# Kernel optimization log

Measured on AMD Instinct MI355X. Metric: run time of the kernel, lower is better.

The kernel has to match this reference:

```python
import jax, jax.numpy as jnp
import numpy as np

B, N, E, H, T, L, NH = 256, 200, 1600, 256, 30, 30, 4
DH = H // NH


def setup_inputs() -> dict:
    key = jax.random.key(0)
    ks = jax.random.split(key, 24)
    s = 0.05
    nrm = lambda k, shape, sc=s: jax.random.normal(k, shape, jnp.float32) * sc
    return {
        'x_feats': nrm(ks[0], (5, B, T, 2), 1.0),
        'node_features': nrm(ks[1], (B, N, 4), 1.0),
        'edge_index': jax.random.randint(ks[2], (B, 2, E), 0, N),
        'gcn_W1': nrm(ks[3], (4, H)),
        'gcn_b1': nrm(ks[4], (H,)),
        'gcn_W2': nrm(ks[5], (H, H)),
        'gcn_b2': nrm(ks[6], (H,)),
        'attn_in_w': nrm(ks[7], (3 * H, H)),
        'attn_in_b': nrm(ks[8], (3 * H,)),
        'attn_out_w': nrm(ks[9], (H, H)),
        'attn_out_b': nrm(ks[10], (H,)),
        'Wih0': nrm(ks[11], (5, 4 * H, 2 + H)),
        'Wih1': nrm(ks[12], (5, 4 * H, H)),
        'Whh': nrm(ks[13], (5, 2, 4 * H, H)),
        'bih': nrm(ks[14], (5, 2, 4 * H)),
        'bhh': nrm(ks[15], (5, 2, 4 * H)),
        'fcW_pv': nrm(ks[16], (2, 2 * L, H)),
        'fcb_pv': nrm(ks[17], (2, 2 * L)),
        'fcW_s': nrm(ks[18], (3, L, H)),
        'fcb_s': nrm(ks[19], (3, L)),
    }


def _lstm2(xin, Wih0, Wih1, Whh, bih, bhh):
    # xin: [B, T, D]; 2-layer LSTM (PyTorch gate order i, f, g, o). Returns last hidden [B, H].
    def run_layer(xt, Wih, Whh_l, b):  # xt: [T, B, D]
        def step(carry, x_t):
            h, c = carry
            z = x_t @ Wih.T + h @ Whh_l.T + b
            i, f, g, o = jnp.split(z, 4, axis=-1)
            c = jax.nn.sigmoid(f) * c + jax.nn.sigmoid(i) * jnp.tanh(g)
            h = jax.nn.sigmoid(o) * jnp.tanh(c)
            return (h, c), h
        z0 = jnp.zeros((xt.shape[1], H), xt.dtype)
        _, ys = jax.lax.scan(step, (z0, z0), xt)
        return ys  # [T, B, H]

    y0 = run_layer(xin.transpose(1, 0, 2), Wih0, Whh[0], bih[0] + bhh[0])
    y1 = run_layer(y0, Wih1, Whh[1], bih[1] + bhh[1])
    return y1[-1]  # [B, H]


def reference(x_feats, node_features, edge_index, gcn_W1, gcn_b1, gcn_W2, gcn_b2,
              attn_in_w, attn_in_b, attn_out_w, attn_out_b,
              Wih0, Wih1, Whh, bih, bhh, fcW_pv, fcb_pv, fcW_s, fcb_s):
    # --- per-graph 2-layer GCN (symmetric-normalized, self-loops), vmapped over batch ---
    def gcn_graph(x, ei):  # x: [N, 4], ei: [2, E]
        ar = jnp.arange(N)
        src = jnp.concatenate([ei[0], ar])
        tgt = jnp.concatenate([ei[1], ar])
        deg = jax.ops.segment_sum(jnp.ones_like(src, dtype=x.dtype), tgt, num_segments=N)
        dinv = jnp.where(deg > 0, jax.lax.rsqrt(deg), 0.0)
        norm = (dinv[src] * dinv[tgt])[:, None]
        def conv(h, W, b):
            m = h @ W
            return jax.ops.segment_sum(norm * m[src], tgt, num_segments=N) + b
        h = jax.nn.relu(conv(x, gcn_W1, gcn_b1))
        return jax.nn.relu(conv(h, gcn_W2, gcn_b2))

    g = jax.vmap(gcn_graph)(node_features, edge_index)  # [B, N, H]

    # --- multi-head self-attention over the N node axis ---
    qkv = g @ attn_in_w.T + attn_in_b  # [B, N, 3H]
    q, k, v = jnp.split(qkv, 3, axis=-1)
    q = q.reshape(B, N, NH, DH)
    k = k.reshape(B, N, NH, DH)
    v = v.reshape(B, N, NH, DH)
    scores = jnp.einsum('bqhd,bkhd->bhqk', q, k) / jnp.sqrt(jnp.asarray(DH, g.dtype))
    attn = jax.nn.softmax(scores, axis=-1)
    o = jnp.einsum('bhqk,bkhd->bqhd', attn, v).reshape(B, N, H)
    o = o @ attn_out_w.T + attn_out_b  # [B, N, H]
    gfeat = o.mean(axis=1)  # mean over node/seq axis -> [B, H]

    # --- broadcast graph context to each timestep, concat with per-branch features ---
    g_rep = jnp.broadcast_to(gfeat[None, :, None, :], (5, B, T, H))
    branch_in = jnp.concatenate([x_feats, g_rep], axis=-1)  # [5, B, T, 2+H]

    # --- 5 branch LSTMs, vmapped over the branch axis ---
    last_h = jax.vmap(_lstm2)(branch_in, Wih0, Wih1, Whh, bih, bhh)  # [5, B, H]

    # --- heads ---
    pv = jnp.einsum('kbh,koh->kbo', last_h[:2], fcW_pv) + fcb_pv[:, None, :]  # [2, B, 2L]
    position_pred = pv[0].reshape(B, L, 2)
    velocity_pred = pv[1].reshape(B, L, 2)
    sot = jnp.einsum('kbh,koh->kbo', last_h[2:], fcW_s) + fcb_s[:, None, :]  # [3, B, L]
    steering_pred = sot[0][..., None]
    object_pred = jax.nn.sigmoid(sot[1])[..., None]
    traffic_pred = jax.nn.sigmoid(sot[2])[..., None]
    # concat heads along last axis: [B, L, 2+2+1+1+1]
    return jnp.concatenate([position_pred, velocity_pred, steering_pred, object_pred, traffic_pred], axis=-1)
```

## Files before the change

### kernel.cpp

```cpp
#include <hip/hip_runtime.h>
#include <hip/hip_bf16.h>

typedef __hip_bfloat16 bf16;
typedef __bf16 bh8 __attribute__((ext_vector_type(8)));
typedef float f32x4 __attribute__((ext_vector_type(4)));

#define BBATCH 256
#define NN   200
#define EE   1600

#define GLOAD16(gp, lp) __builtin_amdgcn_global_load_lds( \
    (const __attribute__((address_space(1))) void*)(gp),  \
    (__attribute__((address_space(3))) void*)(lp), 16, 0, 0)

__device__ inline float bf2f(bf16 v) { return __bfloat162float(v); }
__device__ inline float ldf(const float* p) { return *p; }
__device__ inline float ldf(const bf16* p) { return __bfloat162float(*p); }
__device__ inline void stf(float* p, float v) { *p = v; }
__device__ inline void stf(bf16* p, float v) { *p = __float2bfloat16(v); }

__global__ __launch_bounds__(256) void k_diag(float* out, int n, float v) {
    for (int i = blockIdx.x * 256 + threadIdx.x; i < n; i += gridDim.x * 256) out[i] = v;
}

__global__ __launch_bounds__(256) void k_deg(const int* __restrict__ ei, int* __restrict__ cnt) {
    int idx = blockIdx.x * 256 + threadIdx.x;
    int b = idx / EE, e = idx % EE;
    int tg = ei[(long)b * 2 * EE + EE + e];
    atomicAdd(&cnt[b * NN + tg], 1);
}

__global__ __launch_bounds__(256) void k_dinv(const int* __restrict__ cnt, float* __restrict__ dinv) {
    int i = blockIdx.x * 256 + threadIdx.x;
    dinv[i] = rsqrtf((float)cnt[i] + 1.0f);
}

__global__ __launch_bounds__(256) void k_adj(const int* __restrict__ ei, const float* __restrict__ dinv,
                                             float* __restrict__ AdjF) {
    int idx = blockIdx.x * 256 + threadIdx.x;
    int b = idx / EE, e = idx % EE;
    const int* eb = ei + (long)b * 2 * EE;
    int s = eb[e], tg = eb[EE + e];
    atomicAdd(&AdjF[((long)b * NN + tg) * NN + s], dinv[b * NN + tg] * dinv[b * NN + s]);
}

__global__ __launch_bounds__(256) void k_adjself(const float* __restrict__ dinv, float* __restrict__ AdjF) {
    int idx = blockIdx.x * 256 + threadIdx.x;
    int b = idx / NN, n = idx % NN;
    float d = dinv[idx];
    atomicAdd(&AdjF[((long)b * NN + n) * NN + n], d * d);
}

__global__ __launch_bounds__(256) void k_adjconv(const float* __restrict__ AdjF, bf16* __restrict__ Adjb) {
    long idx = (long)blockIdx.x * 256 + threadIdx.x;
    int col = idx % 224;
    int row = (idx / 224) & 255;
    int b = idx / (224 * 256);
    float v = (row < NN && col < NN) ? AdjF[((long)b * NN + row) * NN + col] : 0.f;
    Adjb[idx] = __float2bfloat16(v);
}

__global__ __launch_bounds__(256) void k_m1t(const float* __restrict__ nf, const float* __restrict__ W1,
                                             bf16* __restrict__ m1t) {
    long idx = (long)blockIdx.x * 256 + threadIdx.x;
    int node = idx % 224;
    int h = (idx / 224) & 255;
    int b = idx / (224 * 256);
    float v = 0.f;
    if (node < NN) {
        const float* x = nf + ((long)b * NN + node) * 4;
        v = x[0] * W1[h] + x[1] * W1[256 + h] + x[2] * W1[512 + h] + x[3] * W1[768 + h];
    }
    m1t[idx] = __float2bfloat16(v);
}

__global__ __launch_bounds__(256) void k_conv(const float* __restrict__ s, bf16* __restrict__ d, int n) {
    int i = blockIdx.x * 256 + threadIdx.x;
    if (i < n) d[i] = __float2bfloat16(s[i]);
}

__global__ __launch_bounds__(256) void k_convT(const float* __restrict__ W2, bf16* __restrict__ w2t) {
    int i = blockIdx.x * 256 + threadIdx.x;
    w2t[i] = __float2bfloat16(W2[((i & 255) << 8) + (i >> 8)]);
}

__global__ __launch_bounds__(256) void k_bsum(const float* __restrict__ bih, const float* __restrict__ bhh,
                                              float* __restrict__ bsum) {
    int i = blockIdx.x * 256 + threadIdx.x;
    bsum[i] = bih[i] + bhh[i];
}

__global__ __launch_bounds__(256) void k_wfrag(const float* __restrict__ Whh, bf16* __restrict__ dst_, int layer) {
    int i = blockIdx.x * 256 + threadIdx.x;
    int lane = i & 63, g = (i >> 6) & 3, kc = (i >> 8) & 7, jw = (i >> 11) & 15, br = i >> 15;
    int row = g * 256 + jw * 16 + (lane & 15);
    int col = kc * 32 + (lane >> 4) * 8;
    const float* src = Whh + (long)(br * 2 + layer) * 262144 + (long)row * 256 + col;
    bf16* dst = dst_ + (long)i * 8;
#pragma unroll
    for (int e = 0; e < 8; ++e) dst[e] = __float2bfloat16(src[e]);
}

template<int BM, int BN, bool RELU, bool CT>
__global__ __launch_bounds__(256)
void mgemm(const bf16* __restrict__ A, long aBatch, int lda,
           const bf16* __restrict__ Bt, long bBatch, int ldb,
           bf16* __restrict__ C, long cBatch, int ldc,
           const float* __restrict__ bias, long biasBatch,
           int K, int Mvalid)
{
    constexpr int ACH = BM / 16, TCH = BM / 16 + BN / 16, PW = TCH / 4;
    constexpr int FM = BM / 32, FN = BN / 32;
    __shared__ bf16 Al[BM][32];
    __shared__ bf16 Bl[BN][32];
    int bz = blockIdx.z;
    const bf16* Ab = A + (long)bz * aBatch + (long)blockIdx.y * BM * lda;
    const bf16* Bb = Bt + (long)bz * bBatch + (long)blockIdx.x * BN * ldb;
    int tid = threadIdx.x, w = tid >> 6, l = tid & 63;
    int wm = w >> 1, wn = w & 1;
    int lrow = l >> 2, lk8 = (l & 3) * 8;
    f32x4 acc[FM][FN] = {};
    for (int k0 = 0; k0 < K; k0 += 32) {
#pragma unroll
        for (int cc = 0; cc < PW; ++cc) {
            int c = w * PW + cc;
            if (c < ACH) GLOAD16(Ab + (long)(c * 16 + lrow) * lda + k0 + lk8, ((char*)&Al[0][0]) + c * 1024);
            else { int bc = c - ACH; GLOAD16(Bb + (long)(bc * 16 + lrow) * ldb + k0 + lk8, ((char*)&Bl[0][0]) + bc * 1024); }
        }
        __syncthreads();
        bh8 af[FM], bfv[FN];
#pragma unroll
        for (int i = 0; i < FM; ++i) af[i] = *(const bh8*)&Al[wm * (BM / 2) + i * 16 + (l & 15)][(l >> 4) * 8];
#pragma unroll
        for (int j = 0; j < FN; ++j) bfv[j] = *(const bh8*)&Bl[wn * (BN / 2) + j * 16 + (l & 15)][(l >> 4) * 8];
#pragma unroll
        for (int i = 0; i < FM; ++i)
#pragma unroll
            for (int j = 0; j < FN; ++j)
                acc[i][j] = __builtin_amdgcn_mfma_f32_16x16x32_bf16(af[i], bfv[j], acc[i][j], 0, 0, 0);
        __syncthreads();
    }
    bf16* Cb = C + (long)bz * cBatch;
    int mq = blockIdx.y * BM + wm * (BM / 2);
    int nq = blockIdx.x * BN + wn * (BN / 2);
#pragma unroll
    for (int i = 0; i < FM; ++i) {
#pragma unroll
        for (int j = 0; j < FN; ++j) {
            int n = nq + j * 16 + (l & 15);
            float bv = bias ? bias[(long)bz * biasBatch + n] : 0.f;
            int m0 = mq + i * 16 + (l >> 4) * 4;
#pragma unroll
            for (int r = 0; r < 4; ++r) {
                int m = m0 + r;
                if (m < Mvalid) {
                    float v = acc[i][j][r] + bv;
                    if (RELU) v = fmaxf(v, 0.f);
                    if (CT) Cb[(long)n * ldc + m] = __float2bfloat16(v);
                    else    Cb[(long)m * ldc + n] = __float2bfloat16(v);
                }
            }
        }
    }
}

__global__ __launch_bounds__(1024)
void k_rnn0(const bf16* __restrict__ wfrag0, const bf16* __restrict__ gpart,
            const float* __restrict__ xf, const float* __restrict__ wih0,
            bf16* __restrict__ y0)
{
    __shared__ bf16 hbuf[2][16][256];
    int g_ = 10 * (blockIdx.x & 7) + (blockIdx.x >> 3);
    int btile = g_ & 15, br = g_ >> 4;
    int tid = threadIdx.x, w = tid >> 6, l = tid & 63;
    int ln = l & 15, lg = l >> 4;
    int j = w * 16 + ln;
    const bf16* wb = wfrag0 + ((long)(br * 16 + w)) * 16384 + l * 8;
    float2 w01[4];
    float gp_c[4][4];
#pragma unroll
    for (int g = 0; g < 4; ++g) {
        w01[g] = *(const float2*)(wih0 + ((long)br * 1024 + g * 256 + j) * 258);
#pragma unroll
        for (int r = 0; r < 4; ++r) {
            int b = btile * 16 + lg * 4 + r;
            gp_c[g][r] = bf2f(gpart[((long)br * 256 + b) * 1024 + g * 256 + j]);
        }
    }
    float c[4] = {};
    int pp = 0;
#pragma unroll 1
    for (int t = 0; t < 30; ++t) {
        f32x4 acc[4] = {};
        if (t > 0) {
            const char* hb = (const char*)hbuf[pp ^ 1];
#pragma unroll
            for (int kc = 0; kc < 8; ++kc) {
                bh8 a = *(const bh8*)(hb + ln * 512 + ((kc * 64 + lg * 16) ^ ((ln & 7) << 4)));
                const bf16* wk = wb + kc * 2048;
#pragma unroll
                for (int g = 0; g < 4; ++g)
                    acc[g] = __builtin_amdgcn_mfma_f32_16x16x32_bf16(a, *(const bh8*)(wk + g * 512), acc[g], 0, 0, 0);
            }
        }
        char* hw = (char*)hbuf[pp];
        float2 xr[4];
#pragma unroll
        for (int r = 0; r < 4; ++r) {
            int b = btile * 16 + lg * 4 + r;
            xr[r] = *(const float2*)(xf + ((long)(br * 256 + b) * 30 + t) * 2);
        }
#pragma unroll
        for (int r = 0; r < 4; ++r) {
            float z[4];
#pragma unroll
            for (int g = 0; g < 4; ++g)
                z[g] = acc[g][r] + gp_c[g][r] + xr[r].x * w01[g].x + xr[r].y * w01[g].y;
            float ig = 1.f / (1.f + __expf(-z[0]));
            float fg = 1.f / (1.f + __expf(-z[1]));
            float gv = 2.f / (1.f + __expf(-2.f * z[2])) - 1.f;
            float og = 1.f / (1.f + __expf(-z[3]));
            float cv = fg * c[r] + ig * gv;
            c[r] = cv;
            float hv = og * (2.f / (1.f + __expf(-2.f * cv)) - 1.f);
            int row = lg * 4 + r;
            *(bf16*)(hw + row * 512 + ((2 * j) ^ ((row & 7) << 4))) = __float2bfloat16(hv);
        }
        __syncthreads();
        {
            int row = tid >> 6;
            int off = (tid & 63) * 8;
            uint2 v = *(const uint2*)(hw + row * 512 + (off ^ ((row & 7) << 4)));
            *(uint2*)((char*)y0 + (((long)(br * 30 + t) * 256 + btile * 16 + row) * 512) + off) = v;
        }
        pp ^= 1;
    }
}

__global__ __launch_bounds__(1024)
void k_rnn1(const bf16* __restrict__ wfrag1, const bf16* __restrict__ zin1,
            bf16* __restrict__ h1out)
{
    __shared__ bf16 hbuf[2][16][256];
    int g_ = 10 * (blockIdx.x & 7) + (blockIdx.x >> 3);
    int btile = g_ & 15, br = g_ >> 4;
    int tid = threadIdx.x, w = tid >> 6, l = tid & 63;
    int ln = l & 15, lg = l >> 4;
    int j = w * 16 + ln;
    const bf16* wb = wfrag1 + ((long)(br * 16 + w)) * 16384 + l * 8;
    float c[4] = {};
    int pp = 0;
    const bf16* zbr = zin1 + (long)br * 7864320;
#pragma unroll 1
    for (int t = 0; t < 30; ++t) {
        float zin[4][4];
#pragma unroll
        for (int r = 0; r < 4; ++r) {
            long mrow = (long)(t * 256 + btile * 16 + lg * 4 + r) * 1024;
#pragma unroll
            for (int g = 0; g < 4; ++g) zin[g][r] = bf2f(zbr[mrow + g * 256 + j]);
        }
        f32x4 acc[4] = {};
        if (t > 0) {
            const char* hb = (const char*)hbuf[pp ^ 1];
#pragma unroll
            for (int kc = 0; kc < 8; ++kc) {
                bh8 a = *(const bh8*)(hb + ln * 512 + ((kc * 64 + lg * 16) ^ ((ln & 7) << 4)));
                const bf16* wk = wb + kc * 2048;
#pragma unroll
                for (int g = 0; g < 4; ++g)
                    acc[g] = __builtin_amdgcn_mfma_f32_16x16x32_bf16(a, *(const bh8*)(wk + g * 512), acc[g], 0, 0, 0);
            }
        }
        char* hw = (char*)hbuf[pp];
#pragma unroll
        for (int r = 0; r < 4; ++r) {
            float z[4];
#pragma unroll
            for (int g = 0; g < 4; ++g) z[g] = acc[g][r] + zin[g][r];
            float ig = 1.f / (1.f + __expf(-z[0]));
            float fg = 1.f / (1.f + __expf(-z[1]));
            float gv = 2.f / (1.f + __expf(-2.f * z[2])) - 1.f;
            float og = 1.f / (1.f + __expf(-z[3]));
            float cv = fg * c[r] + ig * gv;
            c[r] = cv;
            float hv = og * (2.f / (1.f + __expf(-2.f * cv)) - 1.f);
            int row = lg * 4 + r;
            *(bf16*)(hw + row * 512 + ((2 * j) ^ ((row & 7) << 4))) = __float2bfloat16(hv);
            if (t == 29) {
                int b = btile * 16 + row;
                h1out[((long)br * 256 + b) * 256 + j] = __float2bfloat16(hv);
            }
        }
        __syncthreads();
        pp ^= 1;
    }
}

template <bool BT, typename TA, typename TB, typename TC>
__global__ __launch_bounds__(256)
void gemm64(const TA* __restrict__ A, long aBatch, int lda,
            const TB* __restrict__ Bm, long bBatch, int ldb,
            TC* __restrict__ C, long cBatch, int ldc,
            const float* __restrict__ bias, long biasBatch,
            int M, int Nn, int K, int flags) {
    __shared__ float As[16][64];
    __shared__ float Bs[16][64];
    int bz = blockIdx.z;
    const TA* Ab = A + (long)bz * aBatch;
    const TB* Bb = Bm + (long)bz * bBatch;
    TC* Cb = C + (long)bz * cBatch;
    int m0 = blockIdx.y * 64, n0 = blockIdx.x * 64;
    int tid = threadIdx.x;
    int tr = tid >> 4, tc = tid & 15;
    float acc[4][4] = {};
    int la_m = tid >> 2;
    int la_k = (tid & 3) * 4;
    for (int k0 = 0; k0 < K; k0 += 16) {
#pragma unroll
        for (int j = 0; j < 4; ++j) {
            int kk = la_k + j;
            float v = 0.f;
            if (m0 + la_m < M && k0 + kk < K) v = ldf(&Ab[(long)(m0 + la_m) * lda + k0 + kk]);
            As[kk][la_m] = v;
        }
        if (!BT) {
            int n = tid & 63, kb = (tid >> 6) * 4;
#pragma unroll
            for (int j = 0; j < 4; ++j) {
                int kk = kb + j;
                float v = 0.f;
                if (k0 + kk < K && n0 + n < Nn) v = ldf(&Bb[(long)(k0 + kk) * ldb + n0 + n]);
                Bs[kk][n] = v;
            }
        } else {
            int n = tid >> 2, kb = (tid & 3) * 4;
#pragma unroll
            for (int j = 0; j < 4; ++j) {
                int kk = kb + j;
                float v = 0.f;
                if (k0 + kk < K && n0 + n < Nn) v = ldf(&Bb[(long)(n0 + n) * ldb + k0 + kk]);
                Bs[kk][n] = v;
            }
        }
        __syncthreads();
#pragma unroll
        for (int kk = 0; kk < 16; ++kk) {
            float4 a4 = *(const float4*)&As[kk][tr * 4];
            float4 b4 = *(const float4*)&Bs[kk][tc * 4];
            float a[4] = {a4.x, a4.y, a4.z, a4.w};
            float bb[4] = {b4.x, b4.y, b4.z, b4.w};
#pragma unroll
            for (int i = 0; i < 4; ++i)
#pragma unroll
                for (int j = 0; j < 4; ++j) acc[i][j] += a[i] * bb[j];
        }
        __syncthreads();
    }
#pragma unroll
    for (int i = 0; i < 4; ++i) {
        int m = m0 + tr * 4 + i;
        if (m >= M) continue;
#pragma unroll
        for (int j = 0; j < 4; ++j) {
            int n = n0 + tc * 4 + j;
            if (n >= Nn) continue;
            float v = acc[i][j];
            if (bias) v += bias[(long)bz * biasBatch + n];
            if (flags & 1) v = fmaxf(v, 0.f);
            stf(&Cb[(long)m * ldc + n], v);
        }
    }
}

__global__ __launch_bounds__(256) void k_attn(const bf16* __restrict__ qkv, float* __restrict__ gmean) {
    int b = blockIdx.x >> 2, hd = blockIdx.x & 3;
    __shared__ bf16 Ks[208][72];
    __shared__ float CSl[4][208];
    __shared__ float Gp[4][64];
    int tid = threadIdx.x, w = tid >> 6, l = tid & 63;
    const bf16* qb = qkv + (long)b * (NN * 768) + hd * 64;
    for (int i = tid; i < 208 * 8; i += 256) {
        int n = i >> 3, g = i & 7;
        uint4 v = make_uint4(0, 0, 0, 0);
        if (n < NN) v = *(const uint4*)(qb + (long)n * 768 + 256 + g * 8);
        *(uint4*)&Ks[n][g * 8] = v;
    }
    __syncthreads();
    float cs[13];
#pragma unroll
    for (int t = 0; t < 13; ++t) cs[t] = 0.f;
    int ln = l & 15, lg = l >> 4;
    for (int qt = w; qt < 13; qt += 4) {
        int qr = qt * 16 + ln; if (qr > NN - 1) qr = NN - 1;
        bh8 aq0 = *(const bh8*)(qb + (long)qr * 768 + lg * 8);
        bh8 aq1 = *(const bh8*)(qb + (long)qr * 768 + 32 + lg * 8);
        f32x4 s[13];
#pragma unroll
        for (int t = 0; t < 13; ++t) s[t] = f32x4{0.f, 0.f, 0.f, 0.f};
#pragma unroll
        for (int t = 0; t < 13; ++t) {
            bh8 b0 = *(const bh8*)&Ks[t * 16 + ln][lg * 8];
            bh8 b1 = *(const bh8*)&Ks[t * 16 + ln][32 + lg * 8];
            s[t] = __builtin_amdgcn_mfma_f32_16x16x32_bf16(aq0, b0, s[t], 0, 0, 0);
            s[t] = __builtin_amdgcn_mfma_f32_16x16x32_bf16(aq1, b1, s[t], 0, 0, 0);
        }
        float mx[4] = {-1e30f, -1e30f, -1e30f, -1e30f};
#pragma unroll
        for (int t = 0; t < 13; ++t) {
            bool vn = (t < 12) | (ln < 8);
#pragma unroll
            for (int r = 0; r < 4; ++r) {
                float v = s[t][r] * 0.125f;
                s[t][r] = v;
                if (vn) mx[r] = fmaxf(mx[r], v);
            }
        }
#pragma unroll
        for (int off = 1; off < 16; off <<= 1)
#pragma unroll
            for (int r = 0; r < 4; ++r) mx[r] = fmaxf(mx[r], __shfl_xor(mx[r], off));
        float sum[4] = {0.f, 0.f, 0.f, 0.f};
#pragma unroll
        for (int t = 0; t < 13; ++t) {
            bool vn = (t < 12) | (ln < 8);
#pragma unroll
            for (int r = 0; r < 4; ++r) {
                float e = vn ? __expf(s[t][r] - mx[r]) : 0.f;
                s[t][r] = e;
                sum[r] += e;
            }
        }
#pragma unroll
        for (int off = 1; off < 16; off <<= 1)
#pragma unroll
            for (int r = 0; r < 4; ++r) sum[r] += __shfl_xor(sum[r], off);
        float inv[4];
#pragma unroll
        for (int r = 0; r < 4; ++r) inv[r] = 1.f / sum[r];
#pragma unroll
        for (int r = 0; r < 4; ++r) {
            int q = qt * 16 + lg * 4 + r;
            if (q < NN) {
#pragma unroll
                for (int t = 0; t < 13; ++t) cs[t] += s[t][r] * inv[r];
            }
        }
    }
#pragma unroll
    for (int t = 0; t < 13; ++t) {
        cs[t] += __shfl_xor(cs[t], 16);
        cs[t] += __shfl_xor(cs[t], 32);
    }
    if (l < 16) {
#pragma unroll
        for (int t = 0; t < 13; ++t) CSl[w][t * 16 + l] = cs[t];
    }
    __syncthreads();
    float part = 0.f;
    for (int n = w * 50; n < w * 50 + 50; ++n) {
        float csn = CSl[0][n] + CSl[1][n] + CSl[2][n] + CSl[3][n];
        part += csn * bf2f(qb[(long)n * 768 + 512 + l]);
    }
    Gp[w][l] = part;
    __syncthreads();
    if (w == 0) {
        float tot = Gp[0][l] + Gp[1][l] + Gp[2][l] + Gp[3][l];
        gmean[b * 256 + hd * 64 + l] = tot * (1.0f / 200.0f);
    }
}

__global__ __launch_bounds__(256) void k_heads(const bf16* __restrict__ lasth,
                                               const float* __restrict__ fcW_pv, const float* __restrict__ fcb_pv,
                                               const float* __restrict__ fcW_s, const float* __restrict__ fcb_s,
                                               float* __restrict__ out) {
    int b = blockIdx.x;
    __shared__ float hl[5][257];
    for (int idx = threadIdx.x; idx < 5 * 256; idx += 256) {
        int k = idx >> 8, h = idx & 255;
        hl[k][h] = bf2f(lasth[((long)k * 256 + b) * 256 + h]);
    }
    __syncthreads();
    int i = threadIdx.x;
    if (i < 210) {
        int k, o, l, c;
        const float* w;
        float bias;
        bool sig = false;
        if (i < 60)       { k = 0; o = i;       w = fcW_pv + o * 256;        bias = fcb_pv[o];       l = o >> 1; c = o & 1; }
        else if (i < 120) { k = 1; o = i - 60;  w = fcW_pv + (60 + o) * 256; bias = fcb_pv[60 + o];  l = o >> 1; c = 2 + (o & 1); }
        else if (i < 150) { k = 2; o = i - 120; w = fcW_s + o * 256;         bias = fcb_s[o];        l = o; c = 4; }
        else if (i < 180) { k = 3; o = i - 150; w = fcW_s + (30 + o) * 256;  bias = fcb_s[30 + o];   l = o; c = 5; sig = true; }
        else              { k = 4; o = i - 180; w = fcW_s + (60 + o) * 256;  bias = fcb_s[60 + o];   l = o; c = 6; sig = true; }
        float acc = bias;
        for (int h = 0; h < 256; ++h) acc += hl[k][h] * w[h];
        if (sig) acc = 1.f / (1.f + __expf(-acc));
        out[(long)b * 210 + l * 7 + c] = acc;
    }
}

extern "C" void kernel_launch(void* const* d_in, const int* in_sizes, int n_in,
                              void* d_out, int out_size, void* d_ws, size_t ws_size,
                              hipStream_t stream) {
    (void)in_sizes; (void)n_in;
    const float* x_feats   = (const float*)d_in[0];
    const float* node_feat = (const float*)d_in[1];
    const int*   edge_idx  = (const int*)d_in[2];
    const float* gcn_W1    = (const float*)d_in[3];
    const float* gcn_b1    = (const float*)d_in[4];
    const float* gcn_W2    = (const float*)d_in[5];
    const float* gcn_b2    = (const float*)d_in[6];
    const float* attn_in_w = (const float*)d_in[7];
    const float* attn_in_b = (const float*)d_in[8];
    const float* attn_out_w= (const float*)d_in[9];
    const float* attn_out_b= (const float*)d_in[10];
    const float* Wih0      = (const float*)d_in[11];
    const float* Wih1      = (const float*)d_in[12];
    const float* Whh       = (const float*)d_in[13];
    const float* bih       = (const float*)d_in[14];
    const float* bhh       = (const float*)d_in[15];
    const float* fcW_pv    = (const float*)d_in[16];
    const float* fcb_pv    = (const float*)d_in[17];
    const float* fcW_s     = (const float*)d_in[18];
    const float* fcb_s     = (const float*)d_in[19];
    float* out = (float*)d_out;

    const size_t NEEDED = 186966016ULL;
    if (ws_size < NEEDED) {
        k_diag<<<210, 256, 0, stream>>>(out, out_size, (float)(ws_size >> 20));
        return;
    }
    char* base = (char*)d_ws;
    bf16*  Adjb  = (bf16*)(base + 0);
    bf16*  y0    = (bf16*)(base + 0);
    bf16*  m1t   = (bf16*)(base + 29360128);
    bf16*  m2t   = m1t;
    bf16*  actp  = (bf16*)(base + 58720256);
    char*  bigb  = base + 92274688;
    float* AdjF  = (float*)bigb;
    bf16*  qkv   = (bf16*)bigb;
    bf16*  zin1  = (bf16*)bigb;
    bf16*  w2t   = (bf16*)(base + 170917888);
    bf16*  aiwb  = (bf16*)(base + 171048960);
    bf16*  wih1b = (bf16*)(base + 171442176);
    bf16*  wfrag0= (bf16*)(base + 174063616);
    bf16*  wfrag1= (bf16*)(base + 176685056);
    bf16*  gpart = (bf16*)(base + 179306496);
    float* dinv  = (float*)(base + 181927936);
    int*   degc  = (int*)(base + 182132736);
    float* gmean = (float*)(base + 182337536);
    float* gfeat = (float*)(base + 182599680);
    float* bsum  = (float*)(base + 182861824);
    bf16*  h1b   = (bf16*)(base + 186310656);

    hipMemsetAsync(AdjF, 0, 40960000, stream);
    hipMemsetAsync(degc, 0, 204800, stream);

    k_deg<<<1600, 256, 0, stream>>>(edge_idx, degc);
    k_dinv<<<200, 256, 0, stream>>>(degc, dinv);
    k_adj<<<1600, 256, 0, stream>>>(edge_idx, dinv, AdjF);
    k_adjself<<<200, 256, 0, stream>>>(dinv, AdjF);
    k_adjconv<<<57344, 256, 0, stream>>>(AdjF, Adjb);
    k_m1t<<<57344, 256, 0, stream>>>(node_feat, gcn_W1, m1t);

    k_convT<<<256, 256, 0, stream>>>(gcn_W2, w2t);
    k_conv<<<768, 256, 0, stream>>>(attn_in_w, aiwb, 196608);
    k_conv<<<5120, 256, 0, stream>>>(Wih1, wih1b, 1310720);
    k_wfrag<<<640, 256, 0, stream>>>(Whh, wfrag0, 0);
    k_wfrag<<<640, 256, 0, stream>>>(Whh, wfrag1, 1);
    k_bsum<<<40, 256, 0, stream>>>(bih, bhh, bsum);

    mgemm<128, 128, true, false><<<dim3(2, 2, 256), 256, 0, stream>>>(
        Adjb, 57344, 224, m1t, 57344, 224, actp, 65536, 256, gcn_b1, 0, 224, 256);
    mgemm<128, 128, false, true><<<dim3(2, 2, 256), 256, 0, stream>>>(
        actp, 65536, 256, w2t, 0, 256, m2t, 57344, 224, nullptr, 0, 256, 200);
    mgemm<128, 128, true, false><<<dim3(2, 2, 256), 256, 0, stream>>>(
        Adjb, 57344, 224, m2t, 57344, 224, actp, 65536, 256, gcn_b2, 0, 224, 256);
    mgemm<128, 128, false, false><<<dim3(6, 2, 256), 256, 0, stream>>>(
        actp, 65536, 256, aiwb, 0, 256, qkv, 153600, 768, attn_in_b, 0, 256, 200);

    k_attn<<<1024, 256, 0, stream>>>(qkv, gmean);
    gemm64<true, float, float, float><<<dim3(4, 4, 1), 256, 0, stream>>>(
        gmean, 0, 256, attn_out_w, 0, 256, gfeat, 0, 256, attn_out_b, 0, 256, 256, 256, 0);
    gemm64<true, float, float, bf16><<<dim3(16, 4, 5), 256, 0, stream>>>(
        gfeat, 0, 256, Wih0 + 2, 264192, 258, gpart, 262144, 1024, bsum, 2048, 256, 1024, 256, 0);

    k_rnn0<<<80, 1024, 0, stream>>>(wfrag0, gpart, x_feats, Wih0, y0);
    mgemm<128, 128, false, false><<<dim3(8, 60, 5), 256, 0, stream>>>(
        y0, 1966080, 256, wih1b, 262144, 256, zin1, 7864320, 1024, bsum + 1024, 2048, 256, 7680);
    k_rnn1<<<80, 1024, 0, stream>>>(wfrag1, zin1, h1b);
    k_heads<<<256, 256, 0, stream>>>(h1b, fcW_pv, fcb_pv, fcW_s, fcb_s, out);
}
```

Before: 923.4 us.

## Keep recurrent LSTM weights resident in registers and LDS across timesteps

The recurrent weight fragments in both LSTM kernels are now split three ways: half stay in registers, a quarter go to LDS (128 KB dynamic shared memory per block), and the last quarter are still read from global memory each timestep. This cuts the repeated global/L2 traffic for Whh on the 30-step serial path. The input-gate constants are packed as bf16 pairs to make room for the extra registers. The large LDS allocation and higher register pressure may hurt occupancy or cause spilling, and the hipFuncSetAttribute calls add host work on every launch.

```diff
diff --git a/kernel.cpp b/kernel.cpp
--- a/kernel.cpp
+++ b/kernel.cpp
@@ -169,41 +169,77 @@
             const float* __restrict__ xf, const float* __restrict__ wih0,
             bf16* __restrict__ y0)
 {
-    __shared__ bf16 hbuf[2][16][256];
+    extern __shared__ char dyns[];
+    char* wlds = dyns;
+    char* hbase = dyns + 131072;
     int g_ = 10 * (blockIdx.x & 7) + (blockIdx.x >> 3);
     int btile = g_ & 15, br = g_ >> 4;
     int tid = threadIdx.x, w = tid >> 6, l = tid & 63;
     int ln = l & 15, lg = l >> 4;
     int j = w * 16 + ln;
     const bf16* wb = wfrag0 + ((long)(br * 16 + w)) * 16384 + l * 8;
-    float2 w01[4];
-    float gp_c[4][4];
+    bh8 wreg[16];
+#pragma unroll
+    for (int kc = 0; kc < 4; ++kc)
+#pragma unroll
+        for (int g = 0; g < 4; ++g)
+            wreg[kc * 4 + g] = *(const bh8*)(wb + kc * 2048 + g * 512);
+#pragma unroll
+    for (int f = 0; f < 8; ++f) {
+        int kc = 4 + (f >> 2), g = f & 3;
+        *(uint4*)(wlds + (w * 8 + f) * 1024 + l * 16) = *(const uint4*)(wb + kc * 2048 + g * 512);
+    }
+    __hip_bfloat162 w01p[4];
+    __hip_bfloat162 gpk[8];
 #pragma unroll
     for (int g = 0; g < 4; ++g) {
-        w01[g] = *(const float2*)(wih0 + ((long)br * 1024 + g * 256 + j) * 258);
-#pragma unroll
-        for (int r = 0; r < 4; ++r) {
-            int b = btile * 16 + lg * 4 + r;
-            gp_c[g][r] = bf2f(gpart[((long)br * 256 + b) * 1024 + g * 256 + j]);
+        const float* wr = wih0 + ((long)br * 1024 + g * 256 + j) * 258;
+        w01p[g].x = __float2bfloat16(wr[0]);
+        w01p[g].y = __float2bfloat16(wr[1]);
+#pragma unroll
+        for (int rp = 0; rp < 2; ++rp) {
+            int b0 = btile * 16 + lg * 4 + rp * 2;
+            __hip_bfloat162 t2;
+            t2.x = gpart[((long)br * 256 + b0) * 1024 + g * 256 + j];
+            t2.y = gpart[((long)br * 256 + b0 + 1) * 1024 + g * 256 + j];
+            gpk[g * 2 + rp] = t2;
         }
     }
     float c[4] = {};
+    __syncthreads();
     int pp = 0;
 #pragma unroll 1
     for (int t = 0; t < 30; ++t) {
         f32x4 acc[4] = {};
         if (t > 0) {
-            const char* hb = (const char*)hbuf[pp ^ 1];
-#pragma unroll
-            for (int kc = 0; kc < 8; ++kc) {
+            const char* hb = hbase + (pp ^ 1) * 8192;
+#pragma unroll
+            for (int kc = 0; kc < 4; ++kc) {
                 bh8 a = *(const bh8*)(hb + ln * 512 + ((kc * 64 + lg * 16) ^ ((ln & 7) << 4)));
-                const bf16* wk = wb + kc * 2048;
 #pragma unroll
                 for (int g = 0; g < 4; ++g)
-                    acc[g] = __builtin_amdgcn_mfma_f32_16x16x32_bf16(a, *(const bh8*)(wk + g * 512), acc[g], 0, 0, 0);
-            }
-        }
-        char* hw = (char*)hbuf[pp];
+                    acc[g] = __builtin_amdgcn_mfma_f32_16x16x32_bf16(a, wreg[kc * 4 + g], acc[g], 0, 0, 0);
+            }
+#pragma unroll
+            for (int kc = 4; kc < 6; ++kc) {
+                bh8 a = *(const bh8*)(hb + ln * 512 + ((kc * 64 + lg * 16) ^ ((ln & 7) << 4)));
+#pragma unroll
+                for (int g = 0; g < 4; ++g) {
+                    bh8 wv = *(const bh8*)(wlds + (w * 8 + (kc - 4) * 4 + g) * 1024 + l * 16);
+                    acc[g] = __builtin_amdgcn_mfma_f32_16x16x32_bf16(a, wv, acc[g], 0, 0, 0);
+                }
+            }
+#pragma unroll
+            for (int kc = 6; kc < 8; ++kc) {
+                bh8 a = *(const bh8*)(hb + ln * 512 + ((kc * 64 + lg * 16) ^ ((ln & 7) << 4)));
+#pragma unroll
+                for (int g = 0; g < 4; ++g) {
+                    bh8 wv = *(const bh8*)(wb + kc * 2048 + g * 512);
+                    acc[g] = __builtin_amdgcn_mfma_f32_16x16x32_bf16(a, wv, acc[g], 0, 0, 0);
+                }
+            }
+        }
+        char* hw = hbase + pp * 8192;
         float2 xr[4];
 #pragma unroll
         for (int r = 0; r < 4; ++r) {
@@ -214,8 +250,11 @@
         for (int r = 0; r < 4; ++r) {
             float z[4];
 #pragma unroll
-            for (int g = 0; g < 4; ++g)
-                z[g] = acc[g][r] + gp_c[g][r] + xr[r].x * w01[g].x + xr[r].y * w01[g].y;
+            for (int g = 0; g < 4; ++g) {
+                __hip_bfloat162 gp2 = gpk[g * 2 + (r >> 1)];
+                float gpv = (r & 1) ? __high2float(gp2) : __low2float(gp2);
+                z[g] = acc[g][r] + gpv + xr[r].x * __low2float(w01p[g]) + xr[r].y * __high2float(w01p[g]);
+            }
             float ig = 1.f / (1.f + __expf(-z[0]));
             float fg = 1.f / (1.f + __expf(-z[1]));
             float gv = 2.f / (1.f + __expf(-2.f * z[2])) - 1.f;
@@ -241,14 +280,28 @@
 void k_rnn1(const bf16* __restrict__ wfrag1, const bf16* __restrict__ zin1,
             bf16* __restrict__ h1out)
 {
-    __shared__ bf16 hbuf[2][16][256];
+    extern __shared__ char dyns[];
+    char* wlds = dyns;
+    char* hbase = dyns + 131072;
     int g_ = 10 * (blockIdx.x & 7) + (blockIdx.x >> 3);
     int btile = g_ & 15, br = g_ >> 4;
     int tid = threadIdx.x, w = tid >> 6, l = tid & 63;
     int ln = l & 15, lg = l >> 4;
     int j = w * 16 + ln;
     const bf16* wb = wfrag1 + ((long)(br * 16 + w)) * 16384 + l * 8;
+    bh8 wreg[16];
+#pragma unroll
+    for (int kc = 0; kc < 4; ++kc)
+#pragma unroll
+        for (int g = 0; g < 4; ++g)
+            wreg[kc * 4 + g] = *(const bh8*)(wb + kc * 2048 + g * 512);
+#pragma unroll
+    for (int f = 0; f < 8; ++f) {
+        int kc = 4 + (f >> 2), g = f & 3;
+        *(uint4*)(wlds + (w * 8 + f) * 1024 + l * 16) = *(const uint4*)(wb + kc * 2048 + g * 512);
+    }
     float c[4] = {};
+    __syncthreads();
     int pp = 0;
     const bf16* zbr = zin1 + (long)br * 7864320;
 #pragma unroll 1
@@ -262,17 +315,34 @@
         }
         f32x4 acc[4] = {};
         if (t > 0) {
-            const char* hb = (const char*)hbuf[pp ^ 1];
-#pragma unroll
-            for (int kc = 0; kc < 8; ++kc) {
+            const char* hb = hbase + (pp ^ 1) * 8192;
+#pragma unroll
+            for (int kc = 0; kc < 4; ++kc) {
                 bh8 a = *(const bh8*)(hb + ln * 512 + ((kc * 64 + lg * 16) ^ ((ln & 7) << 4)));
-                const bf16* wk = wb + kc * 2048;
 #pragma unroll
                 for (int g = 0; g < 4; ++g)
-                    acc[g] = __builtin_amdgcn_mfma_f32_16x16x32_bf16(a, *(const bh8*)(wk + g * 512), acc[g], 0, 0, 0);
-            }
-        }
-        char* hw = (char*)hbuf[pp];
+                    acc[g] = __builtin_amdgcn_mfma_f32_16x16x32_bf16(a, wreg[kc * 4 + g], acc[g], 0, 0, 0);
+            }
+#pragma unroll
+            for (int kc = 4; kc < 6; ++kc) {
+                bh8 a = *(const bh8*)(hb + ln * 512 + ((kc * 64 + lg * 16) ^ ((ln & 7) << 4)));
+#pragma unroll
+                for (int g = 0; g < 4; ++g) {
+                    bh8 wv = *(const bh8*)(wlds + (w * 8 + (kc - 4) * 4 + g) * 1024 + l * 16);
+                    acc[g] = __builtin_amdgcn_mfma_f32_16x16x32_bf16(a, wv, acc[g], 0, 0, 0);
+                }
+            }
+#pragma unroll
+            for (int kc = 6; kc < 8; ++kc) {
+                bh8 a = *(const bh8*)(hb + ln * 512 + ((kc * 64 + lg * 16) ^ ((ln & 7) << 4)));
+#pragma unroll
+                for (int g = 0; g < 4; ++g) {
+                    bh8 wv = *(const bh8*)(wb + kc * 2048 + g * 512);
+                    acc[g] = __builtin_amdgcn_mfma_f32_16x16x32_bf16(a, wv, acc[g], 0, 0, 0);
+                }
+            }
+        }
+        char* hw = hbase + pp * 8192;
 #pragma unroll
         for (int r = 0; r < 4; ++r) {
             float z[4];
@@ -585,9 +655,11 @@
     gemm64<true, float, float, bf16><<<dim3(16, 4, 5), 256, 0, stream>>>(
         gfeat, 0, 256, Wih0 + 2, 264192, 258, gpart, 262144, 1024, bsum, 2048, 256, 1024, 256, 0);
 
-    k_rnn0<<<80, 1024, 0, stream>>>(wfrag0, gpart, x_feats, Wih0, y0);
+    hipFuncSetAttribute((const void*)k_rnn0, hipFuncAttributeMaxDynamicSharedMemorySize, 147456);
+    hipFuncSetAttribute((const void*)k_rnn1, hipFuncAttributeMaxDynamicSharedMemorySize, 147456);
+    k_rnn0<<<80, 1024, 147456, stream>>>(wfrag0, gpart, x_feats, Wih0, y0);
     mgemm<128, 128, false, false><<<dim3(8, 60, 5), 256, 0, stream>>>(
         y0, 1966080, 256, wih1b, 262144, 256, zin1, 7864320, 1024, bsum + 1024, 2048, 256, 7680);
-    k_rnn1<<<80, 1024, 0, stream>>>(wfrag1, zin1, h1b);
+    k_rnn1<<<80, 1024, 147456, stream>>>(wfrag1, zin1, h1b);
     k_heads<<<256, 256, 0, stream>>>(h1b, fcW_pv, fcb_pv, fcW_s, fcb_s, out);
 }
```

Result: faster. 902.9 us (-2.2%).

## Double-buffer recurrent LSTM weights into LDS via async global-to-LDS loads

Applied to the files above, without the earlier changes.

In both recurrent LSTM kernels, each wave now prefetches the next K-chunk of its Whh fragments into a per-wave double-buffered LDS region with global_load_lds, waiting on vmcnt before reading. This replaces the direct global loads that fed the MFMAs. The goal is to hide global-memory latency inside the serial per-timestep matmul. It moves all LDS to 144KB of dynamic shared memory and adds a launch-bounds occupancy hint. The same weight traffic is still reloaded from global every step. The hand-written vmcnt wait and the tight register hint carry correctness and spill risk.

```diff
diff --git a/kernel.cpp b/kernel.cpp
--- a/kernel.cpp
+++ b/kernel.cpp
@@ -164,18 +164,20 @@
     }
 }
 
-__global__ __launch_bounds__(1024)
+__global__ __launch_bounds__(1024, 4)
 void k_rnn0(const bf16* __restrict__ wfrag0, const bf16* __restrict__ gpart,
             const float* __restrict__ xf, const float* __restrict__ wih0,
             bf16* __restrict__ y0)
 {
-    __shared__ bf16 hbuf[2][16][256];
+    extern __shared__ char dyns[];
+    char* hbase = dyns + 131072;
     int g_ = 10 * (blockIdx.x & 7) + (blockIdx.x >> 3);
     int btile = g_ & 15, br = g_ >> 4;
     int tid = threadIdx.x, w = tid >> 6, l = tid & 63;
     int ln = l & 15, lg = l >> 4;
     int j = w * 16 + ln;
     const bf16* wb = wfrag0 + ((long)(br * 16 + w)) * 16384 + l * 8;
+    char* wsme = dyns + w * 4096;
     float2 w01[4];
     float gp_c[4][4];
 #pragma unroll
@@ -188,22 +190,34 @@
         }
     }
     float c[4] = {};
+#pragma unroll
+    for (int g = 0; g < 4; ++g)
+        GLOAD16(wb + g * 512, wsme + g * 1024);
+    __syncthreads();
     int pp = 0;
 #pragma unroll 1
     for (int t = 0; t < 30; ++t) {
         f32x4 acc[4] = {};
         if (t > 0) {
-            const char* hb = (const char*)hbuf[pp ^ 1];
+            const char* hb = hbase + (pp ^ 1) * 8192;
 #pragma unroll
             for (int kc = 0; kc < 8; ++kc) {
+                int nk = (kc + 1) & 7;
+                int nbuf = (kc + 1) & 1;
+                int cbuf = kc & 1;
+#pragma unroll
+                for (int g = 0; g < 4; ++g)
+                    GLOAD16(wb + nk * 2048 + g * 512, wsme + nbuf * 65536 + g * 1024);
+                asm volatile("s_waitcnt vmcnt(4)" ::: "memory");
                 bh8 a = *(const bh8*)(hb + ln * 512 + ((kc * 64 + lg * 16) ^ ((ln & 7) << 4)));
-                const bf16* wk = wb + kc * 2048;
-#pragma unroll
-                for (int g = 0; g < 4; ++g)
-                    acc[g] = __builtin_amdgcn_mfma_f32_16x16x32_bf16(a, *(const bh8*)(wk + g * 512), acc[g], 0, 0, 0);
-            }
-        }
-        char* hw = (char*)hbuf[pp];
+#pragma unroll
+                for (int g = 0; g < 4; ++g) {
+                    bh8 wv = *(const bh8*)(wsme + cbuf * 65536 + g * 1024 + l * 16);
+                    acc[g] = __builtin_amdgcn_mfma_f32_16x16x32_bf16(a, wv, acc[g], 0, 0, 0);
+                }
+            }
+        }
+        char* hw = hbase + pp * 8192;
         float2 xr[4];
 #pragma unroll
         for (int r = 0; r < 4; ++r) {
@@ -237,18 +251,24 @@
     }
 }
 
-__global__ __launch_bounds__(1024)
+__global__ __launch_bounds__(1024, 4)
 void k_rnn1(const bf16* __restrict__ wfrag1, const bf16* __restrict__ zin1,
             bf16* __restrict__ h1out)
 {
-    __shared__ bf16 hbuf[2][16][256];
+    extern __shared__ char dyns[];
+    char* hbase = dyns + 131072;
     int g_ = 10 * (blockIdx.x & 7) + (blockIdx.x >> 3);
     int btile = g_ & 15, br = g_ >> 4;
     int tid = threadIdx.x, w = tid >> 6, l = tid & 63;
     int ln = l & 15, lg = l >> 4;
     int j = w * 16 + ln;
     const bf16* wb = wfrag1 + ((long)(br * 16 + w)) * 16384 + l * 8;
+    char* wsme = dyns + w * 4096;
     float c[4] = {};
+#pragma unroll
+    for (int g = 0; g < 4; ++g)
+        GLOAD16(wb + g * 512, wsme + g * 1024);
+    __syncthreads();
     int pp = 0;
     const bf16* zbr = zin1 + (long)br * 7864320;
 #pragma unroll 1
@@ -262,17 +282,25 @@
         }
         f32x4 acc[4] = {};
         if (t > 0) {
-            const char* hb = (const char*)hbuf[pp ^ 1];
+            const char* hb = hbase + (pp ^ 1) * 8192;
 #pragma unroll
             for (int kc = 0; kc < 8; ++kc) {
+                int nk = (kc + 1) & 7;
+                int nbuf = (kc + 1) & 1;
+                int cbuf = kc & 1;
+#pragma unroll
+                for (int g = 0; g < 4; ++g)
+                    GLOAD16(wb + nk * 2048 + g * 512, wsme + nbuf * 65536 + g * 1024);
+                asm volatile("s_waitcnt vmcnt(4)" ::: "memory");
                 bh8 a = *(const bh8*)(hb + ln * 512 + ((kc * 64 + lg * 16) ^ ((ln & 7) << 4)));
-                const bf16* wk = wb + kc * 2048;
-#pragma unroll
-                for (int g = 0; g < 4; ++g)
-                    acc[g] = __builtin_amdgcn_mfma_f32_16x16x32_bf16(a, *(const bh8*)(wk + g * 512), acc[g], 0, 0, 0);
-            }
-        }
-        char* hw = (char*)hbuf[pp];
+#pragma unroll
+                for (int g = 0; g < 4; ++g) {
+                    bh8 wv = *(const bh8*)(wsme + cbuf * 65536 + g * 1024 + l * 16);
+                    acc[g] = __builtin_amdgcn_mfma_f32_16x16x32_bf16(a, wv, acc[g], 0, 0, 0);
+                }
+            }
+        }
+        char* hw = hbase + pp * 8192;
 #pragma unroll
         for (int r = 0; r < 4; ++r) {
             float z[4];
@@ -585,9 +613,11 @@
     gemm64<true, float, float, bf16><<<dim3(16, 4, 5), 256, 0, stream>>>(
         gfeat, 0, 256, Wih0 + 2, 264192, 258, gpart, 262144, 1024, bsum, 2048, 256, 1024, 256, 0);
 
-    k_rnn0<<<80, 1024, 0, stream>>>(wfrag0, gpart, x_feats, Wih0, y0);
+    hipFuncSetAttribute((const void*)k_rnn0, hipFuncAttributeMaxDynamicSharedMemorySize, 147456);
+    hipFuncSetAttribute((const void*)k_rnn1, hipFuncAttributeMaxDynamicSharedMemorySize, 147456);
+    k_rnn0<<<80, 1024, 147456, stream>>>(wfrag0, gpart, x_feats, Wih0, y0);
     mgemm<128, 128, false, false><<<dim3(8, 60, 5), 256, 0, stream>>>(
         y0, 1966080, 256, wih1b, 262144, 256, zin1, 7864320, 1024, bsum + 1024, 2048, 256, 7680);
-    k_rnn1<<<80, 1024, 0, stream>>>(wfrag1, zin1, h1b);
+    k_rnn1<<<80, 1024, 147456, stream>>>(wfrag1, zin1, h1b);
     k_heads<<<256, 256, 0, stream>>>(h1b, fcW_pv, fcb_pv, fcW_s, fcb_s, out);
 }
```

Result: slower. 963.9 us (+4.4%).
